# Optimization experiments

Hardware: AMD Instinct MI355X
Metric: run time of the kernel (lower is better)

Reference implementation:

```python
import jax, jax.numpy as jnp
import numpy as np

N_NODES = 100000
N_EDGES = 1600000
DIMS = [128, 128, 128, 128]  # in -> l0 -> l1 -> l2
BN_EPS = 1e-5


def setup_inputs() -> dict:
    key = jax.random.key(0)
    ks = jax.random.split(key, 16)
    inp = {
        "x": jax.random.normal(ks[0], (N_NODES, DIMS[0]), dtype=jnp.float32),
        "edge_index": jax.random.randint(ks[1], (2, N_EDGES), 0, N_NODES, dtype=jnp.int64),
    }
    for i in range(3):
        fan_in, fan_out = DIMS[i], DIMS[i + 1]
        scale = 1.0 / np.sqrt(fan_in)
        inp[f"W{i}"] = jax.random.uniform(ks[2 + 4 * i], (fan_in, fan_out), minval=-scale, maxval=scale, dtype=jnp.float32)
        inp[f"b{i}"] = jnp.zeros((fan_out,), dtype=jnp.float32)
        inp[f"gamma{i}"] = jnp.ones((fan_out,), dtype=jnp.float32)
        inp[f"beta{i}"] = jnp.zeros((fan_out,), dtype=jnp.float32)
    return inp


def _gcn_conv(h, src, dst, dinv_sqrt, W, b):
    # PyG GCNConv: x@W, then symmetric-normalized aggregation with self-loops, then +bias
    hw = h @ W  # [N, out]
    norm = dinv_sqrt[src] * dinv_sqrt[dst]  # [E]
    agg = jax.ops.segment_sum(hw[src] * norm[:, None], dst, num_segments=N_NODES)
    agg = agg + hw * (dinv_sqrt * dinv_sqrt)[:, None]  # self-loop contribution (weight 1/deg)
    return agg + b


def _bn(h, gamma, beta):
    mean = jnp.mean(h, axis=0)
    var = jnp.mean(jnp.square(h - mean), axis=0)  # biased var, as torch BN uses for normalization
    return gamma * (h - mean) * jax.lax.rsqrt(var + BN_EPS) + beta


def reference(x, edge_index, W0, b0, gamma0, beta0, W1, b1, gamma1, beta1, W2, b2, gamma2, beta2):
    src, dst = edge_index[0], edge_index[1]
    # degree with self-loops (edge weight 1), computed once; same adjacency each layer
    deg = jax.ops.segment_sum(jnp.ones((N_EDGES,), dtype=x.dtype), dst, num_segments=N_NODES) + 1.0
    dinv_sqrt = jax.lax.rsqrt(deg)
    h = x
    for W, b, g, be in ((W0, b0, gamma0, beta0), (W1, b1, gamma1, beta1), (W2, b2, gamma2, beta2)):
        h = _gcn_conv(h, src, dst, dinv_sqrt, W, b)
        h = _bn(h, g, be)
        h = jax.nn.relu(h)
    return h
```

## Files before the change

kernel.cpp:

```cpp
#include <hip/hip_runtime.h>
#include <hip/hip_bf16.h>

#define NN 100000
#define NE 1600000
#define BN_EPS 1e-5f
#define NB 391
#define NBKT 782
#define BCAP 512

typedef __attribute__((ext_vector_type(8))) short bf16x8;
typedef __attribute__((ext_vector_type(4))) float f32x4;

static __device__ __forceinline__ ushort f2b(float f) {
  __hip_bfloat16 h = __float2bfloat16(f);
  return __builtin_bit_cast(ushort, h);
}
static __device__ __forceinline__ float blo(uint v) { return __builtin_bit_cast(float, v << 16); }
static __device__ __forceinline__ float bhi(uint v) { return __builtin_bit_cast(float, v & 0xFFFF0000u); }

__global__ __launch_bounds__(256) void k_bin(const int* __restrict__ ei, int* __restrict__ deg,
                                             int* __restrict__ bfill, uint* __restrict__ binned) {
  const int e = blockIdx.x * 256 + threadIdx.x;
  const int s = ei[e];
  const int d = ei[NE + e];
  atomicAdd(&deg[d], 1);
  const int bucket = d >> 7;
  const int idx = (blockIdx.x & 7) * NBKT + bucket;
  const int pos = atomicAdd(&bfill[idx], 1);
  binned[(size_t)idx * BCAP + pos] = ((uint)(d & 127) << 17) | (uint)s;
}

__global__ __launch_bounds__(256) void k_dinv(const int* __restrict__ deg, float* __restrict__ dinv) {
  int v = blockIdx.x * 256 + threadIdx.x;
  if (v < NN) dinv[v] = rsqrtf((float)deg[v] + 1.0f);
}

__global__ __launch_bounds__(256) void k_scan1(const int* __restrict__ deg, int* __restrict__ bsum) {
  __shared__ int lds[256];
  const int t = threadIdx.x;
  const int i = blockIdx.x * 256 + t;
  lds[t] = (i < NN) ? deg[i] : 0;
  __syncthreads();
  for (int d = 128; d > 0; d >>= 1) {
    if (t < d) lds[t] += lds[t + d];
    __syncthreads();
  }
  if (t == 0) bsum[blockIdx.x] = lds[0];
}

__global__ __launch_bounds__(512) void k_scan2(const int* __restrict__ bsum, int* __restrict__ boff,
                                               int* __restrict__ rp) {
  __shared__ int lds[512];
  const int t = threadIdx.x;
  const int own = (t < NB) ? bsum[t] : 0;
  lds[t] = own;
  __syncthreads();
  for (int d = 1; d < 512; d <<= 1) {
    int v = (t >= d) ? lds[t - d] : 0;
    __syncthreads();
    lds[t] += v;
    __syncthreads();
  }
  if (t < NB) boff[t] = lds[t] - own;
  if (t == 511) rp[NN] = lds[511];
}

__global__ __launch_bounds__(256) void k_scan3(const int* __restrict__ deg, const int* __restrict__ boff,
                                               int* __restrict__ rp) {
  __shared__ int lds[256];
  const int t = threadIdx.x;
  const int i = blockIdx.x * 256 + t;
  const int own = (i < NN) ? deg[i] : 0;
  lds[t] = own;
  __syncthreads();
  for (int d = 1; d < 256; d <<= 1) {
    int v = (t >= d) ? lds[t - d] : 0;
    __syncthreads();
    lds[t] += v;
    __syncthreads();
  }
  if (i < NN) rp[i] = boff[blockIdx.x] + lds[t] - own;
}

__global__ __launch_bounds__(256) void k_scatter2(const uint* __restrict__ binned,
                                                  const int* __restrict__ bfill,
                                                  const int* __restrict__ rp, int* __restrict__ csr) {
  __shared__ int lfill[128];
  __shared__ int lrp[128];
  const int t = threadIdx.x;
  const int bucket = blockIdx.x;
  const int v0 = bucket << 7;
  if (t < 128) {
    lfill[t] = 0;
    lrp[t] = (v0 + t < NN) ? rp[v0 + t] : 0;
  }
  __syncthreads();
  #pragma unroll
  for (int r = 0; r < 8; ++r) {
    const int idx = r * NBKT + bucket;
    const int c = bfill[idx];
    const uint* seg = binned + (size_t)idx * BCAP;
    for (int j = t; j < c; j += 256) {
      const uint u = seg[j];
      const int ld = u >> 17;
      const int s = (int)(u & 0x1FFFFu);
      const int pos = lrp[ld] + atomicAdd(&lfill[ld], 1);
      csr[pos] = s;
    }
  }
}

__global__ __launch_bounds__(128) void k_wt(const float* __restrict__ W0, const float* __restrict__ W1,
                                            const float* __restrict__ W2, ushort* __restrict__ wt) {
  const int lay = blockIdx.y, n = blockIdx.x, k = threadIdx.x;
  const float* W = (lay == 0) ? W0 : (lay == 1) ? W1 : W2;
  wt[lay * 16384 + n * 128 + k] = f2b(W[k * 128 + n]);
}

__global__ __launch_bounds__(256) void k_gemm(const float* __restrict__ hf,
                                              const ushort* __restrict__ wt,
                                              const float* __restrict__ sc, const float* __restrict__ sh,
                                              const int aff,
                                              ushort* __restrict__ hw) {
  __shared__ ushort wlds[128 * 128];
  __shared__ float scs[128], shs[128];
  const int t = threadIdx.x;
  {
    const uint4* src = (const uint4*)wt;
    uint4* dst = (uint4*)wlds;
    #pragma unroll
    for (int i = 0; i < 8; ++i) {
      int idx = t + i * 256;
      int n = idx >> 4;
      dst[idx ^ (n & 7)] = src[idx];
    }
  }
  if (t < 128) { scs[t] = aff ? sc[t] : 1.0f; shs[t] = aff ? sh[t] : 0.0f; }
  __syncthreads();

  const int wv = t >> 6, l = t & 63;
  const int lr = l & 15, lk = l >> 4;
  const int row0 = blockIdx.x * 128 + wv * 32;
  f32x4 acc[2][8] = {};
  const uint4* wchunks = (const uint4*)wlds;

  #pragma unroll
  for (int kb = 0; kb < 4; ++kb) {
    const int k0 = kb * 32 + lk * 8;
    const float4 s4a = *(const float4*)(scs + k0);
    const float4 s4b = *(const float4*)(scs + k0 + 4);
    const float4 h4a = *(const float4*)(shs + k0);
    const float4 h4b = *(const float4*)(shs + k0 + 4);
    const int r0 = min(row0 + lr, NN - 1);
    const int r1 = min(row0 + 16 + lr, NN - 1);
    bf16x8 a0, a1;
    #pragma unroll
    for (int rr = 0; rr < 2; ++rr) {
      const int r = rr ? r1 : r0;
      const float4 p = *(const float4*)(hf + (size_t)r * 128 + k0);
      const float4 q = *(const float4*)(hf + (size_t)r * 128 + k0 + 4);
      float u0 = fmaf(s4a.x, p.x, h4a.x), u1 = fmaf(s4a.y, p.y, h4a.y);
      float u2 = fmaf(s4a.z, p.z, h4a.z), u3 = fmaf(s4a.w, p.w, h4a.w);
      float u4 = fmaf(s4b.x, q.x, h4b.x), u5 = fmaf(s4b.y, q.y, h4b.y);
      float u6 = fmaf(s4b.z, q.z, h4b.z), u7 = fmaf(s4b.w, q.w, h4b.w);
      if (aff) {
        u0 = fmaxf(u0, 0.f); u1 = fmaxf(u1, 0.f); u2 = fmaxf(u2, 0.f); u3 = fmaxf(u3, 0.f);
        u4 = fmaxf(u4, 0.f); u5 = fmaxf(u5, 0.f); u6 = fmaxf(u6, 0.f); u7 = fmaxf(u7, 0.f);
      }
      bf16x8 a;
      a[0] = (short)f2b(u0); a[1] = (short)f2b(u1); a[2] = (short)f2b(u2); a[3] = (short)f2b(u3);
      a[4] = (short)f2b(u4); a[5] = (short)f2b(u5); a[6] = (short)f2b(u6); a[7] = (short)f2b(u7);
      if (rr) a1 = a; else a0 = a;
    }
    #pragma unroll
    for (int nt = 0; nt < 8; ++nt) {
      const int n = nt * 16 + lr;
      const int chunk = n * 16 + ((kb * 4 + lk) ^ (n & 7));
      const bf16x8 b = *(const bf16x8*)(wchunks + chunk);
      acc[0][nt] = __builtin_amdgcn_mfma_f32_16x16x32_bf16(a0, b, acc[0][nt], 0, 0, 0);
      acc[1][nt] = __builtin_amdgcn_mfma_f32_16x16x32_bf16(a1, b, acc[1][nt], 0, 0, 0);
    }
  }
  #pragma unroll
  for (int rt = 0; rt < 2; ++rt)
    #pragma unroll
    for (int j = 0; j < 4; ++j) {
      const int row = row0 + rt * 16 + lk * 4 + j;
      if (row < NN) {
        #pragma unroll
        for (int nt = 0; nt < 8; ++nt)
          hw[(size_t)row * 128 + nt * 16 + lr] = f2b(acc[rt][nt][j]);
      }
    }
}

__global__ __launch_bounds__(256) void k_agg(const ushort* __restrict__ hw,
                                             const int* __restrict__ rp, const int* __restrict__ csr,
                                             const float* __restrict__ dinv, const float* __restrict__ bias,
                                             float* __restrict__ out) {
  const int wid = (blockIdx.x * 256 + threadIdx.x) >> 6;
  const int lane = threadIdx.x & 63;
  const int v = wid;
  const int beg = rp[v], end = rp[v + 1];
  float ax = 0.f, ay = 0.f;
  int i = beg;
  for (; i + 8 <= end; i += 8) {
    int s[8]; float dd[8]; uint w[8];
    #pragma unroll
    for (int j = 0; j < 8; ++j) s[j] = csr[i + j];
    #pragma unroll
    for (int j = 0; j < 8; ++j) dd[j] = dinv[s[j]];
    #pragma unroll
    for (int j = 0; j < 8; ++j) w[j] = *(const uint*)(hw + (size_t)s[j] * 128 + 2 * lane);
    #pragma unroll
    for (int j = 0; j < 8; ++j) {
      ax = fmaf(dd[j], blo(w[j]), ax);
      ay = fmaf(dd[j], bhi(w[j]), ay);
    }
  }
  for (; i + 4 <= end; i += 4) {
    const int s0 = csr[i], s1 = csr[i + 1], s2 = csr[i + 2], s3 = csr[i + 3];
    const float d0 = dinv[s0], d1 = dinv[s1], d2 = dinv[s2], d3 = dinv[s3];
    const uint v0 = *(const uint*)(hw + (size_t)s0 * 128 + 2 * lane);
    const uint v1 = *(const uint*)(hw + (size_t)s1 * 128 + 2 * lane);
    const uint v2 = *(const uint*)(hw + (size_t)s2 * 128 + 2 * lane);
    const uint v3 = *(const uint*)(hw + (size_t)s3 * 128 + 2 * lane);
    ax = fmaf(d0, blo(v0), ax); ay = fmaf(d0, bhi(v0), ay);
    ax = fmaf(d1, blo(v1), ax); ay = fmaf(d1, bhi(v1), ay);
    ax = fmaf(d2, blo(v2), ax); ay = fmaf(d2, bhi(v2), ay);
    ax = fmaf(d3, blo(v3), ax); ay = fmaf(d3, bhi(v3), ay);
  }
  for (; i < end; ++i) {
    const int s = csr[i];
    const float ds = dinv[s];
    const uint vv = *(const uint*)(hw + (size_t)s * 128 + 2 * lane);
    ax = fmaf(ds, blo(vv), ax); ay = fmaf(ds, bhi(vv), ay);
  }
  const float dv = dinv[v];
  const uint sv = *(const uint*)(hw + (size_t)v * 128 + 2 * lane);
  const float bx = bias[2 * lane], by = bias[2 * lane + 1];
  float2 o;
  o.x = fmaf(ax, dv, fmaf(blo(sv), dv * dv, bx));
  o.y = fmaf(ay, dv, fmaf(bhi(sv), dv * dv, by));
  *(float2*)(out + (size_t)v * 128 + 2 * lane) = o;
}

__global__ __launch_bounds__(256) void k_bnstats(const float* __restrict__ h, float* __restrict__ stats) {
  __shared__ float rs[256], rs2[256];
  const int t = threadIdx.x;
  const int col = t & 127, rg = t >> 7;
  const int row0 = blockIdx.x * 128;
  const int rend = min(row0 + 128, NN);
  float s = 0.f, s2 = 0.f;
  for (int r = row0 + rg; r < rend; r += 2) {
    float v = h[(size_t)r * 128 + col];
    s += v;
    s2 = fmaf(v, v, s2);
  }
  rs[t] = s; rs2[t] = s2;
  __syncthreads();
  if (t < 128) {
    atomicAdd(&stats[t], rs[t] + rs[t + 128]);
    atomicAdd(&stats[128 + t], rs2[t] + rs2[t + 128]);
  }
}

__global__ void k_bnfin(const float* __restrict__ stats, const float* __restrict__ gamma,
                        const float* __restrict__ beta, float* __restrict__ sc, float* __restrict__ sh) {
  const int c = threadIdx.x;
  const float inv_n = 1.0f / (float)NN;
  const float mean = stats[c] * inv_n;
  const float var = fmaxf(stats[128 + c] * inv_n - mean * mean, 0.f);
  const float k = gamma[c] * rsqrtf(var + BN_EPS);
  sc[c] = k;
  sh[c] = fmaf(-mean, k, beta[c]);
}

__global__ __launch_bounds__(256) void k_bnfinal(float* __restrict__ h,
                                                 const float* __restrict__ sc, const float* __restrict__ sh) {
  const int i = blockIdx.x * 256 + threadIdx.x;
  const int c = (i & 31) * 4;
  float4 v = ((const float4*)h)[i];
  v.x = fmaxf(fmaf(sc[c + 0], v.x, sh[c + 0]), 0.f);
  v.y = fmaxf(fmaf(sc[c + 1], v.y, sh[c + 1]), 0.f);
  v.z = fmaxf(fmaf(sc[c + 2], v.z, sh[c + 2]), 0.f);
  v.w = fmaxf(fmaf(sc[c + 3], v.w, sh[c + 3]), 0.f);
  ((float4*)h)[i] = v;
}

extern "C" void kernel_launch(void* const* d_in, const int* in_sizes, int n_in,
                              void* d_out, int out_size, void* d_ws, size_t ws_size,
                              hipStream_t stream) {
  const float* x  = (const float*)d_in[0];
  const int*   ei = (const int*)d_in[1];
  const float* W[3]  = {(const float*)d_in[2],  (const float*)d_in[6],  (const float*)d_in[10]};
  const float* b[3]  = {(const float*)d_in[3],  (const float*)d_in[7],  (const float*)d_in[11]};
  const float* g[3]  = {(const float*)d_in[4],  (const float*)d_in[8],  (const float*)d_in[12]};
  const float* be[3] = {(const float*)d_in[5],  (const float*)d_in[9],  (const float*)d_in[13]};

  char* ws = (char*)d_ws;
  ushort* hwb    = (ushort*)(ws);
  uint*   binned = (uint*)(ws);
  int*    bfill  = (int*)(ws + 13000000);
  int*    csr    = (int*)(ws + 51200000);
  int*    deg    = (int*)(ws + 57600000);
  int*    rp     = (int*)(ws + 58000000);
  float*  dinv   = (float*)(ws + 58400016);
  ushort* wtb    = (ushort*)(ws + 58800016);
  float*  stats  = (float*)(ws + 58898320);
  float*  sc     = (float*)(ws + 58899344);
  float*  sh     = (float*)(ws + 58899856);
  int*    bsum   = (int*)(ws + 58900368);
  int*    boff   = (int*)(ws + 58901936);
  float*  hbuf   = (float*)d_out;

  hipMemsetAsync(deg, 0, NN * 4, stream);
  hipMemsetAsync(bfill, 0, 8 * NBKT * 4, stream);
  k_bin<<<NE / 256, 256, 0, stream>>>(ei, deg, bfill, binned);
  k_dinv<<<(NN + 255) / 256, 256, 0, stream>>>(deg, dinv);
  k_scan1<<<NB, 256, 0, stream>>>(deg, bsum);
  k_scan2<<<1, 512, 0, stream>>>(bsum, boff, rp);
  k_scan3<<<NB, 256, 0, stream>>>(deg, boff, rp);
  k_scatter2<<<NBKT, 256, 0, stream>>>(binned, bfill, rp, csr);
  k_wt<<<dim3(128, 3), 128, 0, stream>>>(W[0], W[1], W[2], wtb);

  for (int L = 0; L < 3; ++L) {
    const float* hin = (L == 0) ? x : hbuf;
    k_gemm<<<(NN + 127) / 128, 256, 0, stream>>>(hin, wtb + L * 16384, sc, sh, (L > 0) ? 1 : 0, hwb);
    k_agg<<<25000, 256, 0, stream>>>(hwb, rp, csr, dinv, b[L], hbuf);
    hipMemsetAsync(stats, 0, 256 * 4, stream);
    k_bnstats<<<(NN + 127) / 128, 256, 0, stream>>>(hbuf, stats);
    k_bnfin<<<1, 128, 0, stream>>>(stats, g[L], be[L], sc, sh);
  }
  k_bnfinal<<<NN * 128 / 1024, 256, 0, stream>>>(hbuf, sc, sh);
}
```

Baseline: 662.5 us.

## Rebuild CSR construction with block-local histogram binning into 1024-node buckets

Replaces per-edge global atomics in binning with a per-block shared-memory histogram that reserves global ranges once per bucket. Degree counting moves into a separate pass over the binned buckets using LDS atomics, and the scatter now uses 98 buckets of 1024 destinations each. The aggregation loop also gains a 16-wide unrolled gather stage in place of the 4-wide stage. The coarser buckets use only 98 blocks for the deg and scatter kernels, which may underuse the GPU, and the binned data must fit in the fixed 18432-entry bucket capacity.

```diff
diff --git a/kernel.cpp b/kernel.cpp
--- a/kernel.cpp
+++ b/kernel.cpp
@@ -5,8 +5,8 @@
 #define NE 1600000
 #define BN_EPS 1e-5f
 #define NB 391
-#define NBKT 782
-#define BCAP 512
+#define NBKT2 98
+#define BCAP2 18432
 
 typedef __attribute__((ext_vector_type(8))) short bf16x8;
 typedef __attribute__((ext_vector_type(4))) float f32x4;
@@ -18,16 +18,48 @@
 static __device__ __forceinline__ float blo(uint v) { return __builtin_bit_cast(float, v << 16); }
 static __device__ __forceinline__ float bhi(uint v) { return __builtin_bit_cast(float, v & 0xFFFF0000u); }
 
-__global__ __launch_bounds__(256) void k_bin(const int* __restrict__ ei, int* __restrict__ deg,
-                                             int* __restrict__ bfill, uint* __restrict__ binned) {
-  const int e = blockIdx.x * 256 + threadIdx.x;
-  const int s = ei[e];
-  const int d = ei[NE + e];
-  atomicAdd(&deg[d], 1);
-  const int bucket = d >> 7;
-  const int idx = (blockIdx.x & 7) * NBKT + bucket;
-  const int pos = atomicAdd(&bfill[idx], 1);
-  binned[(size_t)idx * BCAP + pos] = ((uint)(d & 127) << 17) | (uint)s;
+__global__ __launch_bounds__(256) void k_bin2(const int* __restrict__ ei, int* __restrict__ gfill,
+                                              uint* __restrict__ binned) {
+  __shared__ int hist[NBKT2], lfill[NBKT2], gpos[NBKT2];
+  const int t = threadIdx.x;
+  const int base = blockIdx.x * 4096;
+  if (t < NBKT2) { hist[t] = 0; lfill[t] = 0; }
+  __syncthreads();
+  int s[16], d[16];
+  #pragma unroll
+  for (int j = 0; j < 16; ++j) {
+    const int e = base + j * 256 + t;
+    if (e < NE) { s[j] = ei[e]; d[j] = ei[NE + e]; }
+    else d[j] = -1;
+  }
+  #pragma unroll
+  for (int j = 0; j < 16; ++j)
+    if (d[j] >= 0) atomicAdd(&hist[d[j] >> 10], 1);
+  __syncthreads();
+  if (t < NBKT2) gpos[t] = atomicAdd(&gfill[t], hist[t]);
+  __syncthreads();
+  #pragma unroll
+  for (int j = 0; j < 16; ++j)
+    if (d[j] >= 0) {
+      const int b = d[j] >> 10;
+      const int pos = gpos[b] + atomicAdd(&lfill[b], 1);
+      binned[(size_t)b * BCAP2 + pos] = ((uint)(d[j] & 1023) << 17) | (uint)s[j];
+    }
+}
+
+__global__ __launch_bounds__(1024) void k_deg(const uint* __restrict__ binned,
+                                              const int* __restrict__ gfill, int* __restrict__ deg) {
+  __shared__ int lcnt[1024];
+  const int t = threadIdx.x;
+  const int b = blockIdx.x;
+  lcnt[t] = 0;
+  __syncthreads();
+  const int c = gfill[b];
+  const uint* seg = binned + (size_t)b * BCAP2;
+  for (int j = t; j < c; j += 1024) atomicAdd(&lcnt[seg[j] >> 17], 1);
+  __syncthreads();
+  const int v = b * 1024 + t;
+  if (v < NN) deg[v] = lcnt[t];
 }
 
 __global__ __launch_bounds__(256) void k_dinv(const int* __restrict__ deg, float* __restrict__ dinv) {
@@ -82,31 +114,23 @@
   if (i < NN) rp[i] = boff[blockIdx.x] + lds[t] - own;
 }
 
-__global__ __launch_bounds__(256) void k_scatter2(const uint* __restrict__ binned,
-                                                  const int* __restrict__ bfill,
-                                                  const int* __restrict__ rp, int* __restrict__ csr) {
-  __shared__ int lfill[128];
-  __shared__ int lrp[128];
-  const int t = threadIdx.x;
-  const int bucket = blockIdx.x;
-  const int v0 = bucket << 7;
-  if (t < 128) {
-    lfill[t] = 0;
-    lrp[t] = (v0 + t < NN) ? rp[v0 + t] : 0;
-  }
-  __syncthreads();
-  #pragma unroll
-  for (int r = 0; r < 8; ++r) {
-    const int idx = r * NBKT + bucket;
-    const int c = bfill[idx];
-    const uint* seg = binned + (size_t)idx * BCAP;
-    for (int j = t; j < c; j += 256) {
-      const uint u = seg[j];
-      const int ld = u >> 17;
-      const int s = (int)(u & 0x1FFFFu);
-      const int pos = lrp[ld] + atomicAdd(&lfill[ld], 1);
-      csr[pos] = s;
-    }
+__global__ __launch_bounds__(1024) void k_scatter3(const uint* __restrict__ binned,
+                                                   const int* __restrict__ gfill,
+                                                   const int* __restrict__ rp, int* __restrict__ csr) {
+  __shared__ int lrp[1024], lfill[1024];
+  const int t = threadIdx.x;
+  const int b = blockIdx.x;
+  const int v = b * 1024 + t;
+  lrp[t] = (v < NN) ? rp[v] : 0;
+  lfill[t] = 0;
+  __syncthreads();
+  const int c = gfill[b];
+  const uint* seg = binned + (size_t)b * BCAP2;
+  for (int j = t; j < c; j += 1024) {
+    const uint u = seg[j];
+    const int d10 = u >> 17;
+    const int pos = lrp[d10] + atomicAdd(&lfill[d10], 1);
+    csr[pos] = (int)(u & 0x1FFFFu);
   }
 }
 
@@ -204,6 +228,20 @@
   const int beg = rp[v], end = rp[v + 1];
   float ax = 0.f, ay = 0.f;
   int i = beg;
+  for (; i + 16 <= end; i += 16) {
+    int s[16]; float dd[16]; uint w[16];
+    #pragma unroll
+    for (int j = 0; j < 16; ++j) s[j] = csr[i + j];
+    #pragma unroll
+    for (int j = 0; j < 16; ++j) dd[j] = dinv[s[j]];
+    #pragma unroll
+    for (int j = 0; j < 16; ++j) w[j] = *(const uint*)(hw + (size_t)s[j] * 128 + 2 * lane);
+    #pragma unroll
+    for (int j = 0; j < 16; ++j) {
+      ax = fmaf(dd[j], blo(w[j]), ax);
+      ay = fmaf(dd[j], bhi(w[j]), ay);
+    }
+  }
   for (; i + 8 <= end; i += 8) {
     int s[8]; float dd[8]; uint w[8];
     #pragma unroll
@@ -217,18 +255,6 @@
       ax = fmaf(dd[j], blo(w[j]), ax);
       ay = fmaf(dd[j], bhi(w[j]), ay);
     }
-  }
-  for (; i + 4 <= end; i += 4) {
-    const int s0 = csr[i], s1 = csr[i + 1], s2 = csr[i + 2], s3 = csr[i + 3];
-    const float d0 = dinv[s0], d1 = dinv[s1], d2 = dinv[s2], d3 = dinv[s3];
-    const uint v0 = *(const uint*)(hw + (size_t)s0 * 128 + 2 * lane);
-    const uint v1 = *(const uint*)(hw + (size_t)s1 * 128 + 2 * lane);
-    const uint v2 = *(const uint*)(hw + (size_t)s2 * 128 + 2 * lane);
-    const uint v3 = *(const uint*)(hw + (size_t)s3 * 128 + 2 * lane);
-    ax = fmaf(d0, blo(v0), ax); ay = fmaf(d0, bhi(v0), ay);
-    ax = fmaf(d1, blo(v1), ax); ay = fmaf(d1, bhi(v1), ay);
-    ax = fmaf(d2, blo(v2), ax); ay = fmaf(d2, bhi(v2), ay);
-    ax = fmaf(d3, blo(v3), ax); ay = fmaf(d3, bhi(v3), ay);
   }
   for (; i < end; ++i) {
     const int s = csr[i];
@@ -301,7 +327,6 @@
   char* ws = (char*)d_ws;
   ushort* hwb    = (ushort*)(ws);
   uint*   binned = (uint*)(ws);
-  int*    bfill  = (int*)(ws + 13000000);
   int*    csr    = (int*)(ws + 51200000);
   int*    deg    = (int*)(ws + 57600000);
   int*    rp     = (int*)(ws + 58000000);
@@ -312,16 +337,17 @@
   float*  sh     = (float*)(ws + 58899856);
   int*    bsum   = (int*)(ws + 58900368);
   int*    boff   = (int*)(ws + 58901936);
+  int*    gfill  = (int*)(ws + 58903504);
   float*  hbuf   = (float*)d_out;
 
-  hipMemsetAsync(deg, 0, NN * 4, stream);
-  hipMemsetAsync(bfill, 0, 8 * NBKT * 4, stream);
-  k_bin<<<NE / 256, 256, 0, stream>>>(ei, deg, bfill, binned);
+  hipMemsetAsync(gfill, 0, NBKT2 * 4, stream);
+  k_bin2<<<(NE + 4095) / 4096, 256, 0, stream>>>(ei, gfill, binned);
+  k_deg<<<NBKT2, 1024, 0, stream>>>(binned, gfill, deg);
   k_dinv<<<(NN + 255) / 256, 256, 0, stream>>>(deg, dinv);
   k_scan1<<<NB, 256, 0, stream>>>(deg, bsum);
   k_scan2<<<1, 512, 0, stream>>>(bsum, boff, rp);
   k_scan3<<<NB, 256, 0, stream>>>(deg, boff, rp);
-  k_scatter2<<<NBKT, 256, 0, stream>>>(binned, bfill, rp, csr);
+  k_scatter3<<<NBKT2, 1024, 0, stream>>>(binned, gfill, rp, csr);
   k_wt<<<dim3(128, 3), 128, 0, stream>>>(W[0], W[1], W[2], wtb);
 
   for (int L = 0; L < 3; ++L) {
```

New measurement: 667.9 us. Within noise of the previous version (+0.8%).
